# Optimization experiments

Measured on AMD Instinct MI355X. Metric: run time of the kernel, lower is better.

Reference implementation:

```python
import jax, jax.numpy as jnp
import numpy as np

N_NODES = 50000
N_EDGES = 800000
IN_CH, HID, OUT_CH = 128, 256, 40


def setup_inputs() -> dict:
    key = jax.random.key(0)
    ks = jax.random.split(key, 10)
    x = jax.random.normal(ks[0], (N_NODES, IN_CH), dtype=jnp.float32)
    edge_index = jax.random.randint(ks[1], (2, N_EDGES), 0, N_NODES, dtype=jnp.int64)
    s = 0.05  # weight init scale
    return {
        "x": x,
        "edge_index": edge_index,
        "W1a": jax.random.normal(ks[2], (IN_CH, HID), dtype=jnp.float32) * s,
        "b1a": jnp.zeros((HID,), jnp.float32),
        "W2a": jax.random.normal(ks[3], (HID, HID), dtype=jnp.float32) * s,
        "b2a": jnp.zeros((HID,), jnp.float32),
        "W1b": jax.random.normal(ks[4], (HID, HID), dtype=jnp.float32) * s,
        "b1b": jnp.zeros((HID,), jnp.float32),
        "W2b": jax.random.normal(ks[5], (HID, HID), dtype=jnp.float32) * s,
        "b2b": jnp.zeros((HID,), jnp.float32),
        "Wlin": jax.random.normal(ks[6], (HID * 2, OUT_CH), dtype=jnp.float32) * s,
        "blin": jnp.zeros((OUT_CH,), jnp.float32),
    }


def _gin_conv(h, src, dst, W1, b1, W2, b2):
    # sum-aggregate messages h[src] into destination nodes, eps = 0
    agg = jax.ops.segment_sum(h[src], dst, num_segments=N_NODES)
    z = h + agg
    z = jnp.maximum(z @ W1 + b1, 0.0) @ W2 + b2  # 2-layer MLP
    return z


def reference(x, edge_index, W1a, b1a, W2a, b2a, W1b, b1b, W2b, b2b, Wlin, blin):
    src, dst = edge_index[0], edge_index[1]
    h1 = jnp.maximum(_gin_conv(x, src, dst, W1a, b1a, W2a, b2a), 0.0)
    h2 = jnp.maximum(_gin_conv(h1, src, dst, W1b, b1b, W2b, b2b), 0.0)
    h_cat = jnp.concatenate([h1, h2], axis=1)  # [N, 2*HID]
    logits = h_cat @ Wlin + blin
    return jax.nn.log_softmax(logits, axis=1)
```

## Files before the change

### kernel.cpp

```cpp
#include <hip/hip_runtime.h>
#include <math.h>

#define N_NODES 50000
#define N_EDGES 800000
#define IN_CH 128
#define HID 256
#define OUT_CH 40
#define GRP 6250
#define NCHUNK 64
#define TS 264

typedef unsigned short u16;
typedef unsigned char u8;
typedef __attribute__((ext_vector_type(8))) short bf16x8;
typedef __attribute__((ext_vector_type(8))) unsigned short u16x8;
typedef __attribute__((ext_vector_type(4))) float f32x4;
typedef __attribute__((ext_vector_type(2))) float f32x2;

__device__ __forceinline__ float bf2f(u16 u) {
    union { unsigned int i; float f; } v; v.i = ((unsigned int)u) << 16; return v.f;
}
__device__ __forceinline__ u16 f2bf(float f) {
    union { float f; unsigned int i; } v; v.f = f;
    unsigned int x = v.i;
    x += 0x7fffu + ((x >> 16) & 1u);
    return (u16)(x >> 16);
}

#define GLOBAL_AS __attribute__((address_space(1)))
#define LDS_AS __attribute__((address_space(3)))
__device__ __forceinline__ void async_cp16(const void* g, void* l) {
    __builtin_amdgcn_global_load_lds((const GLOBAL_AS unsigned int*)g,
                                     (LDS_AS unsigned int*)l, 16, 0, 0);
}

__device__ __forceinline__ void pack_w(
    const float* __restrict__ in, u16* __restrict__ out, int K, int N, int c)
{
    for (int k = threadIdx.x; k < K; k += 256) {
        int kk32 = k >> 5, quad = (k >> 3) & 3, e = k & 7;
        size_t base = (((size_t)c * (K >> 5) + kk32) * 64 + quad * 16) * 8 + e;
#pragma unroll
        for (int li = 0; li < 16; li++) {
            int n = c * 16 + li;
            float v = (n < N) ? in[(size_t)k * N + n] : 0.f;
            out[base + (size_t)li * 8] = f2bf(v);
        }
    }
}

__global__ __launch_bounds__(256) void prep_fused(
    const float* __restrict__ x, u16* __restrict__ xb, u8* __restrict__ xf8,
    const int* __restrict__ ei, u16* __restrict__ e16,
    const float* __restrict__ W1a, const float* __restrict__ W2a,
    const float* __restrict__ W1b, const float* __restrict__ W2b,
    const float* __restrict__ Wlin,
    u16* __restrict__ W1aPk, u16* __restrict__ W2aPk,
    u16* __restrict__ W1bPk, u16* __restrict__ W2bPk, u16* __restrict__ WlinPk)
{
    int b = blockIdx.x;
    if (b < 6250) {
        int i = b * 256 + threadIdx.x;
        float4 v = ((const float4*)x)[i];
        ushort4 o;
        o.x = f2bf(v.x); o.y = f2bf(v.y); o.z = f2bf(v.z); o.w = f2bf(v.w);
        ((ushort4*)xb)[i] = o;
        int p = __builtin_amdgcn_cvt_pk_fp8_f32(v.x, v.y, 0, false);
        p = __builtin_amdgcn_cvt_pk_fp8_f32(v.z, v.w, p, true);
        ((unsigned int*)xf8)[i] = (unsigned int)p;
    } else if (b < 7813) {
        int i = (b - 6250) * 256 + threadIdx.x;
        if (i < (2 * N_EDGES) / 4) {
            int4 v = ((const int4*)ei)[i];
            ushort4 o;
            o.x = (u16)v.x; o.y = (u16)v.y; o.z = (u16)v.z; o.w = (u16)v.w;
            ((ushort4*)e16)[i] = o;
        }
    } else {
        int t = b - 7813;
        if (t < 16)       pack_w(W1a, W1aPk, IN_CH, HID, t);
        else if (t < 32)  pack_w(W2a, W2aPk, HID, HID, t - 16);
        else if (t < 48)  pack_w(W1b, W1bPk, HID, HID, t - 32);
        else if (t < 64)  pack_w(W2b, W2bPk, HID, HID, t - 48);
        else              pack_w(Wlin, WlinPk, 2 * HID, OUT_CH, t - 64);
    }
}

__global__ __launch_bounds__(256) void hist_priv(
    const u16* __restrict__ dst16, u16* __restrict__ partial)
{
    __shared__ int hist[GRP];
    const int b = blockIdx.x;
    const int g = b & 7;
    const int sub = b >> 3;
    const int lo = g * GRP;
    const int CH = N_EDGES / NCHUNK;
    for (int i = threadIdx.x; i < GRP; i += 256) hist[i] = 0;
    __syncthreads();
    const ushort4* dsts = (const ushort4*)(dst16 + sub * CH);
    for (int k = threadIdx.x; k < CH / 4; k += 256) {
        ushort4 d = dsts[k];
        int r0 = (int)d.x - lo, r1 = (int)d.y - lo;
        int r2 = (int)d.z - lo, r3 = (int)d.w - lo;
        if ((unsigned)r0 < (unsigned)GRP) atomicAdd(&hist[r0], 1);
        if ((unsigned)r1 < (unsigned)GRP) atomicAdd(&hist[r1], 1);
        if ((unsigned)r2 < (unsigned)GRP) atomicAdd(&hist[r2], 1);
        if ((unsigned)r3 < (unsigned)GRP) atomicAdd(&hist[r3], 1);
    }
    __syncthreads();
    u16* po = partial + (size_t)b * GRP;
    for (int i = threadIdx.x; i < GRP; i += 256) po[i] = (u16)hist[i];
}

__global__ __launch_bounds__(256) void scan1(
    const u16* __restrict__ partial, int* __restrict__ excl,
    int* __restrict__ partials_out)
{
    __shared__ int lds[256];
    const int tid = threadIdx.x;
    const int base = blockIdx.x * 1024 + tid * 4;
    int v[4]; int s = 0;
#pragma unroll
    for (int i = 0; i < 4; i++) {
        int idx = base + i;
        int d = 0;
        if (idx < N_NODES) {
            int g = idx / GRP;
            int off = idx - g * GRP;
#pragma unroll
            for (int sub = 0; sub < NCHUNK; sub++)
                d += partial[(size_t)(sub * 8 + g) * GRP + off];
        }
        v[i] = d;
        s += d;
    }
    lds[tid] = s;
    __syncthreads();
    for (int off = 1; off < 256; off <<= 1) {
        int t = (tid >= off) ? lds[tid - off] : 0;
        __syncthreads();
        lds[tid] += t;
        __syncthreads();
    }
    int run = lds[tid] - s;
#pragma unroll
    for (int i = 0; i < 4; i++) {
        int idx = base + i;
        if (idx < N_NODES) excl[idx] = run;
        run += v[i];
    }
    if (tid == 255) partials_out[blockIdx.x] = lds[255];
}

__global__ __launch_bounds__(256) void scan3(
    int* __restrict__ excl, const int* __restrict__ partials,
    int* __restrict__ cursor, int nPart)
{
    __shared__ int bp[64];
    const int tid = threadIdx.x;
    if (tid < 64) {
        int orig = (tid < nPart) ? partials[tid] : 0;
        int v = orig;
#pragma unroll
        for (int off = 1; off < 64; off <<= 1) {
            int t = __shfl_up(v, off, 64);
            if (tid >= off) v += t;
        }
        bp[tid] = v - orig;
    }
    __syncthreads();
    int idx = blockIdx.x * 256 + tid;
    if (idx < N_NODES) {
        int r = excl[idx] + bp[idx >> 10];
        excl[idx] = r;
        cursor[idx] = r;
    }
}

__global__ __launch_bounds__(256) void csr_fill(
    const u16* __restrict__ src16, const u16* __restrict__ dst16,
    int* __restrict__ cursor, u16* __restrict__ csr_src)
{
    const int g = blockIdx.x & 7;
    const int c = blockIdx.x >> 3;
    const int lo = g * GRP, hi = lo + GRP;
    const int base = c * 2048;
#pragma unroll
    for (int i = 0; i < 8; i++) {
        int e = base + i * 256 + threadIdx.x;
        if (e < N_EDGES) {
            int d = dst16[e];
            if (d >= lo && d < hi) {
                int pos = atomicAdd(&cursor[d], 1);
                csr_src[pos] = src16[e];
            }
        }
    }
}

__global__ __launch_bounds__(256) void gather_agg_f8_128(
    const u16* __restrict__ feat_bf, const u8* __restrict__ feat_f8,
    const int* __restrict__ row_ptr, const int* __restrict__ row_end,
    const u16* __restrict__ csr_src, u16* __restrict__ out)
{
    int node = (blockIdx.x * 256 + threadIdx.x) >> 6;
    int lane = threadIdx.x & 63;
    if (node >= N_NODES) return;
    ushort2 sv = ((const ushort2*)(feat_bf + (size_t)node * IN_CH))[lane];
    float ax = bf2f(sv.x), ay = bf2f(sv.y);
    int j = row_ptr[node], e = row_end[node];
    for (; j + 4 <= e; j += 4) {
        int s0 = csr_src[j], s1 = csr_src[j + 1];
        int s2 = csr_src[j + 2], s3 = csr_src[j + 3];
        int v0 = ((const u16*)(feat_f8 + (size_t)s0 * IN_CH))[lane];
        int v1 = ((const u16*)(feat_f8 + (size_t)s1 * IN_CH))[lane];
        int v2 = ((const u16*)(feat_f8 + (size_t)s2 * IN_CH))[lane];
        int v3 = ((const u16*)(feat_f8 + (size_t)s3 * IN_CH))[lane];
        f32x2 d0 = __builtin_amdgcn_cvt_pk_f32_fp8(v0, false);
        f32x2 d1 = __builtin_amdgcn_cvt_pk_f32_fp8(v1, false);
        f32x2 d2 = __builtin_amdgcn_cvt_pk_f32_fp8(v2, false);
        f32x2 d3 = __builtin_amdgcn_cvt_pk_f32_fp8(v3, false);
        ax += (d0.x + d1.x) + (d2.x + d3.x);
        ay += (d0.y + d1.y) + (d2.y + d3.y);
    }
    for (; j < e; j++) {
        int sa = csr_src[j];
        int va = ((const u16*)(feat_f8 + (size_t)sa * IN_CH))[lane];
        f32x2 da = __builtin_amdgcn_cvt_pk_f32_fp8(va, false);
        ax += da.x; ay += da.y;
    }
    ushort2 o; o.x = f2bf(ax); o.y = f2bf(ay);
    ((ushort2*)(out + (size_t)node * IN_CH))[lane] = o;
}

__global__ __launch_bounds__(256) void gather_agg_f8_256(
    const u16* __restrict__ feat_bf, const u8* __restrict__ feat_f8,
    const int* __restrict__ row_ptr, const int* __restrict__ row_end,
    const u16* __restrict__ csr_src, u16* __restrict__ out)
{
    int node = (blockIdx.x * 256 + threadIdx.x) >> 6;
    int lane = threadIdx.x & 63;
    if (node >= N_NODES) return;
    ushort4 sv = ((const ushort4*)(feat_bf + (size_t)node * HID))[lane];
    float ax = bf2f(sv.x), ay = bf2f(sv.y), az = bf2f(sv.z), aw = bf2f(sv.w);
    int j = row_ptr[node], e = row_end[node];
    for (; j + 4 <= e; j += 4) {
        int s0 = csr_src[j], s1 = csr_src[j + 1];
        int s2 = csr_src[j + 2], s3 = csr_src[j + 3];
        int v0 = ((const int*)(feat_f8 + (size_t)s0 * HID))[lane];
        int v1 = ((const int*)(feat_f8 + (size_t)s1 * HID))[lane];
        int v2 = ((const int*)(feat_f8 + (size_t)s2 * HID))[lane];
        int v3 = ((const int*)(feat_f8 + (size_t)s3 * HID))[lane];
        f32x2 l0 = __builtin_amdgcn_cvt_pk_f32_fp8(v0, false);
        f32x2 h0 = __builtin_amdgcn_cvt_pk_f32_fp8(v0, true);
        f32x2 l1 = __builtin_amdgcn_cvt_pk_f32_fp8(v1, false);
        f32x2 h1v = __builtin_amdgcn_cvt_pk_f32_fp8(v1, true);
        f32x2 l2 = __builtin_amdgcn_cvt_pk_f32_fp8(v2, false);
        f32x2 h2v = __builtin_amdgcn_cvt_pk_f32_fp8(v2, true);
        f32x2 l3 = __builtin_amdgcn_cvt_pk_f32_fp8(v3, false);
        f32x2 h3 = __builtin_amdgcn_cvt_pk_f32_fp8(v3, true);
        ax += (l0.x + l1.x) + (l2.x + l3.x);
        ay += (l0.y + l1.y) + (l2.y + l3.y);
        az += (h0.x + h1v.x) + (h2v.x + h3.x);
        aw += (h0.y + h1v.y) + (h2v.y + h3.y);
    }
    for (; j < e; j++) {
        int sa = csr_src[j];
        int va = ((const int*)(feat_f8 + (size_t)sa * HID))[lane];
        f32x2 la = __builtin_amdgcn_cvt_pk_f32_fp8(va, false);
        f32x2 ha = __builtin_amdgcn_cvt_pk_f32_fp8(va, true);
        ax += la.x; ay += la.y; az += ha.x; aw += ha.y;
    }
    ushort4 o;
    o.x = f2bf(ax); o.y = f2bf(ay); o.z = f2bf(az); o.w = f2bf(aw);
    ((ushort4*)(out + (size_t)node * HID))[lane] = o;
}

__global__ __launch_bounds__(256, 4) void mlp_fused(
    const u16* __restrict__ A, int K1,
    const u16* __restrict__ W1pk, const float* __restrict__ b1,
    const u16* __restrict__ W2pk, const float* __restrict__ b2,
    u16* __restrict__ out, u8* __restrict__ outF8, int M)
{
    __shared__ u16 SB[64 * TS];

    const int tid = threadIdx.x;
    const int lane = tid & 63;
    const int wid = tid >> 6;
    const int li = lane & 15;
    const int quad = lane >> 4;
    const int koff = quad * 8;
    const int row0 = blockIdx.x * 64;
    const int KB1 = K1 >> 5;
    const int rsh = (K1 == 256) ? 9 : 8;

    {
        const u8* Ag = (const u8*)(A + (size_t)row0 * K1);
        const int rounds = K1 >> 5;
        for (int j = 0; j < rounds; j++) {
            int L = (j * 256 + tid) * 16;
            int G = L ^ (((L >> rsh) & 7) << 4);
            async_cp16(Ag + G, (u8*)SB + L);
        }
    }

    f32x4 acc[4][4];
#pragma unroll
    for (int i = 0; i < 4; i++)
#pragma unroll
        for (int j = 0; j < 4; j++) acc[i][j] = (f32x4){0.f, 0.f, 0.f, 0.f};

    __syncthreads();

    for (int kk = 0; kk < K1; kk += 32) {
        const int kk32 = kk >> 5;
        bf16x8 af[4], wf[4];
#pragma unroll
        for (int t = 0; t < 4; t++) {
            int row = t * 16 + li;
            int bo = row * (K1 * 2) + (kk + koff) * 2;
            bo ^= (row & 7) << 4;
            af[t] = *(const bf16x8*)((const u8*)SB + bo);
        }
#pragma unroll
        for (int t = 0; t < 4; t++)
            wf[t] = *(const bf16x8*)(W1pk +
                (((size_t)(wid * 4 + t) * KB1 + kk32) * 64 + lane) * 8);
#pragma unroll
        for (int mt = 0; mt < 4; mt++)
#pragma unroll
            for (int nt = 0; nt < 4; nt++)
                acc[mt][nt] = __builtin_amdgcn_mfma_f32_16x16x32_bf16(
                    af[mt], wf[nt], acc[mt][nt], 0, 0, 0);
    }
    __syncthreads();

#pragma unroll
    for (int nt = 0; nt < 4; nt++) {
        int col = wid * 64 + nt * 16 + li;
        float bv = b1[col];
#pragma unroll
        for (int mt = 0; mt < 4; mt++) {
#pragma unroll
            for (int reg = 0; reg < 4; reg++) {
                int row = mt * 16 + quad * 4 + reg;
                float v = fmaxf(acc[mt][nt][reg] + bv, 0.f);
                SB[row * TS + col] = f2bf(v);
                acc[mt][nt][reg] = 0.f;
            }
        }
    }
    __syncthreads();

    for (int kk = 0; kk < HID; kk += 32) {
        const int kk32 = kk >> 5;
        bf16x8 af[4], wf[4];
#pragma unroll
        for (int t = 0; t < 4; t++)
            af[t] = *(const bf16x8*)(SB + (t * 16 + li) * TS + kk + koff);
#pragma unroll
        for (int t = 0; t < 4; t++)
            wf[t] = *(const bf16x8*)(W2pk +
                (((size_t)(wid * 4 + t) * 8 + kk32) * 64 + lane) * 8);
#pragma unroll
        for (int mt = 0; mt < 4; mt++)
#pragma unroll
            for (int nt = 0; nt < 4; nt++)
                acc[mt][nt] = __builtin_amdgcn_mfma_f32_16x16x32_bf16(
                    af[mt], wf[nt], acc[mt][nt], 0, 0, 0);
    }

    __syncthreads();
#pragma unroll
    for (int nt = 0; nt < 4; nt++) {
        int col = wid * 64 + nt * 16 + li;
        float bv = b2[col];
#pragma unroll
        for (int mt = 0; mt < 4; mt++) {
#pragma unroll
            for (int reg = 0; reg < 4; reg++) {
                int row = mt * 16 + quad * 4 + reg;
                float v = fmaxf(acc[mt][nt][reg] + bv, 0.f);
                SB[row * TS + col] = f2bf(v);
            }
        }
    }
    __syncthreads();
#pragma unroll
    for (int it = 0; it < 8; it++) {
        int flat = it * 4096 + tid * 16;
        int r = flat >> 9;
        int cu = (flat & 511) >> 1;
        int row = row0 + r;
        if (row < M) {
            u16x8 v = *(const u16x8*)(SB + r * TS + cu);
            *(u16x8*)(out + (size_t)row * HID + cu) = v;
            if (outF8 != nullptr) {
                int p0 = __builtin_amdgcn_cvt_pk_fp8_f32(bf2f(v[0]), bf2f(v[1]), 0, false);
                p0 = __builtin_amdgcn_cvt_pk_fp8_f32(bf2f(v[2]), bf2f(v[3]), p0, true);
                int p1 = __builtin_amdgcn_cvt_pk_fp8_f32(bf2f(v[4]), bf2f(v[5]), 0, false);
                p1 = __builtin_amdgcn_cvt_pk_fp8_f32(bf2f(v[6]), bf2f(v[7]), p1, true);
                int2 pv; pv.x = p0; pv.y = p1;
                *(int2*)(outF8 + (size_t)row * HID + cu) = pv;
            }
        }
    }
}

__global__ __launch_bounds__(256, 6) void gemm_mfma(
    const u16* __restrict__ A, const u16* __restrict__ Acat, int Ksplit, int ldA,
    const u16* __restrict__ Bpk, const float* __restrict__ bias,
    float* __restrict__ out, int M, int K)
{
    const int tid = threadIdx.x;
    const int lane = tid & 63;
    const int wid = tid >> 6;
    const int li = lane & 15;
    const int quad = lane >> 4;
    const int koff = quad * 8;
    const int row0 = blockIdx.x * 64 + wid * 16;

    f32x4 acc[3];
#pragma unroll
    for (int i = 0; i < 3; i++) acc[i] = (f32x4){0.f, 0.f, 0.f, 0.f};

    int r = row0 + li;
    const int arow = (r < M) ? r : (M - 1);
    const int KB = K >> 5;

#define LD_G(AF, BF, KK)                                                      \
    {   const u16* Ab = ((KK) >= Ksplit) ? Acat : A;                          \
        const int kb = ((KK) >= Ksplit) ? ((KK) - Ksplit) : (KK);             \
        AF = *(const bf16x8*)(Ab + (size_t)arow * ldA + kb + koff);           \
        _Pragma("unroll")                                                     \
        for (int t = 0; t < 3; t++)                                           \
            BF[t] = *(const bf16x8*)(Bpk +                                    \
                (((size_t)t * KB + ((KK) >> 5)) * 64 + lane) * 8); }
#define MFMA3(AF, BF)                                                         \
    {   _Pragma("unroll")                                                     \
        for (int nt = 0; nt < 3; nt++)                                        \
            acc[nt] = __builtin_amdgcn_mfma_f32_16x16x32_bf16(                \
                AF, BF[nt], acc[nt], 0, 0, 0); }

    {
        bf16x8 a0, b0[3], a1, b1v[3];
        LD_G(a0, b0, 0);
        for (int kk = 0; kk < K; kk += 64) {
            LD_G(a1, b1v, kk + 32);
            MFMA3(a0, b0);
            if (kk + 64 < K) LD_G(a0, b0, kk + 64);
            MFMA3(a1, b1v);
        }
    }
#undef LD_G
#undef MFMA3

    float b0v = bias[li];
    float b1s = bias[16 + li];
    float b2s = (li < 8) ? bias[32 + li] : 0.f;
#pragma unroll
    for (int reg = 0; reg < 4; reg++) {
        int row = row0 + quad * 4 + reg;
        float v0 = acc[0][reg] + b0v;
        float v1 = acc[1][reg] + b1s;
        float v2 = (li < 8) ? (acc[2][reg] + b2s) : -INFINITY;
        float m = fmaxf(fmaxf(v0, v1), v2);
#pragma unroll
        for (int off = 1; off < 16; off <<= 1)
            m = fmaxf(m, __shfl_xor(m, off, 64));
        float s = expf(v0 - m) + expf(v1 - m)
                + ((li < 8) ? expf(v2 - m) : 0.f);
#pragma unroll
        for (int off = 1; off < 16; off <<= 1)
            s += __shfl_xor(s, off, 64);
        float lg = m + logf(s);
        if (row < M) {
            out[(size_t)row * OUT_CH + li] = v0 - lg;
            out[(size_t)row * OUT_CH + 16 + li] = v1 - lg;
            if (li < 8) out[(size_t)row * OUT_CH + 32 + li] = v2 - lg;
        }
    }
}

extern "C" void kernel_launch(void* const* d_in, const int* in_sizes, int n_in,
                              void* d_out, int out_size, void* d_ws, size_t ws_size,
                              hipStream_t stream)
{
    const float* x    = (const float*)d_in[0];
    const int*   ei   = (const int*)d_in[1];
    const float* W1a  = (const float*)d_in[2];
    const float* b1a  = (const float*)d_in[3];
    const float* W2a  = (const float*)d_in[4];
    const float* b2a  = (const float*)d_in[5];
    const float* W1b  = (const float*)d_in[6];
    const float* b1b  = (const float*)d_in[7];
    const float* W2b  = (const float*)d_in[8];
    const float* b2b  = (const float*)d_in[9];
    const float* Wlin = (const float*)d_in[10];
    const float* blin = (const float*)d_in[11];
    float* out = (float*)d_out;

    const size_t R = (size_t)N_NODES * HID;
    u16* R0 = (u16*)d_ws;
    u16* R1 = R0 + R;
    u16* R2 = R1 + R;
    u16* R3 = R2 + R;
    u16* R4 = R3 + R;
    u16* xbf = R0;
    u16* zA  = R1;
    u16* partial = (u16*)R1;
    u8*  xf8 = (u8*)(R1 + (size_t)N_NODES * IN_CH);
    u8*  h1f8 = (u8*)R1;
    u16* h1  = R3;
    u16* zB  = R4;
    u16* h2  = R2;

    u16* wts = R4 + R;
    u16* W1aPk = wts;
    u16* W2aPk = W1aPk + 256 * 128;
    u16* W1bPk = W2aPk + 256 * 256;
    u16* W2bPk = W1bPk + 256 * 256;
    u16* WlinPk = W2bPk + 256 * 256;
    int* rowp   = (int*)(WlinPk + 128 * 512);
    int* cursor = rowp + N_NODES;
    int* part   = cursor + N_NODES;
    u16* csr    = (u16*)(part + 64);
    u16* e16    = csr + N_EDGES;
    u16* src16  = e16;
    u16* dst16  = e16 + N_EDGES;

    dim3 blk(256);
    const int scanBlocks = (N_NODES + 1023) / 1024;
    const int aggBlocks  = (N_NODES + 3) / 4;
    const int fillBlocks = 8 * ((N_EDGES + 2047) / 2048);
    const int mlpBlocks  = (N_NODES + 63) / 64;
    const int gemmBlocks = (N_NODES + 63) / 64;

    prep_fused<<<7880, blk, 0, stream>>>(x, xbf, xf8, ei, e16,
                                         W1a, W2a, W1b, W2b, Wlin,
                                         W1aPk, W2aPk, W1bPk, W2bPk, WlinPk);
    hist_priv<<<8 * NCHUNK, blk, 0, stream>>>(dst16, partial);
    scan1<<<scanBlocks, blk, 0, stream>>>(partial, rowp, part);
    scan3<<<(N_NODES + 255) / 256, blk, 0, stream>>>(rowp, part, cursor, scanBlocks);
    csr_fill<<<fillBlocks, blk, 0, stream>>>(src16, dst16, cursor, csr);

    gather_agg_f8_128<<<aggBlocks, blk, 0, stream>>>(xbf, xf8, rowp, cursor, csr, zA);
    mlp_fused<<<mlpBlocks, blk, 0, stream>>>(zA, IN_CH, W1aPk, b1a, W2aPk, b2a,
                                             h1, h1f8, N_NODES);

    gather_agg_f8_256<<<aggBlocks, blk, 0, stream>>>(h1, h1f8, rowp, cursor, csr, zB);
    mlp_fused<<<mlpBlocks, blk, 0, stream>>>(zB, HID, W1bPk, b1b, W2bPk, b2b,
                                             h2, nullptr, N_NODES);

    gemm_mfma<<<gemmBlocks, blk, 0, stream>>>(h1, h2, HID, HID, WlinPk, blin,
                                              out, N_NODES, 2 * HID);
}
```

Baseline: 301.5 us.

## Pack multiple nodes per wavefront in gather-aggregate with wide 16-byte loads

The gather kernels previously gave each node a full 64-lane wave, with each lane reading 2 or 4 bytes per neighbor row. Now each wave handles 8 nodes (128-ch) or 4 nodes (256-ch), and each lane loads 16 fp8 bytes with int4 loads and keeps 16 accumulators. Loops run to the max degree within the wave, with masked loads for shorter rows. The goal is fewer, wider memory transactions and more nodes in flight. The cost is more registers and divergence from uneven degrees across nodes sharing a wave.

```diff
diff --git a/kernel.cpp b/kernel.cpp
--- a/kernel.cpp
+++ b/kernel.cpp
@@ -198,39 +198,63 @@
     }
 }
 
+
 __global__ __launch_bounds__(256) void gather_agg_f8_128(
     const u16* __restrict__ feat_bf, const u8* __restrict__ feat_f8,
     const int* __restrict__ row_ptr, const int* __restrict__ row_end,
     const u16* __restrict__ csr_src, u16* __restrict__ out)
 {
-    int node = (blockIdx.x * 256 + threadIdx.x) >> 6;
-    int lane = threadIdx.x & 63;
-    if (node >= N_NODES) return;
-    ushort2 sv = ((const ushort2*)(feat_bf + (size_t)node * IN_CH))[lane];
-    float ax = bf2f(sv.x), ay = bf2f(sv.y);
-    int j = row_ptr[node], e = row_end[node];
-    for (; j + 4 <= e; j += 4) {
-        int s0 = csr_src[j], s1 = csr_src[j + 1];
-        int s2 = csr_src[j + 2], s3 = csr_src[j + 3];
-        int v0 = ((const u16*)(feat_f8 + (size_t)s0 * IN_CH))[lane];
-        int v1 = ((const u16*)(feat_f8 + (size_t)s1 * IN_CH))[lane];
-        int v2 = ((const u16*)(feat_f8 + (size_t)s2 * IN_CH))[lane];
-        int v3 = ((const u16*)(feat_f8 + (size_t)s3 * IN_CH))[lane];
-        f32x2 d0 = __builtin_amdgcn_cvt_pk_f32_fp8(v0, false);
-        f32x2 d1 = __builtin_amdgcn_cvt_pk_f32_fp8(v1, false);
-        f32x2 d2 = __builtin_amdgcn_cvt_pk_f32_fp8(v2, false);
-        f32x2 d3 = __builtin_amdgcn_cvt_pk_f32_fp8(v3, false);
-        ax += (d0.x + d1.x) + (d2.x + d3.x);
-        ay += (d0.y + d1.y) + (d2.y + d3.y);
-    }
-    for (; j < e; j++) {
-        int sa = csr_src[j];
-        int va = ((const u16*)(feat_f8 + (size_t)sa * IN_CH))[lane];
-        f32x2 da = __builtin_amdgcn_cvt_pk_f32_fp8(va, false);
-        ax += da.x; ay += da.y;
-    }
-    ushort2 o; o.x = f2bf(ax); o.y = f2bf(ay);
-    ((ushort2*)(out + (size_t)node * IN_CH))[lane] = o;
+    const int tid = threadIdx.x;
+    const int lane = tid & 63;
+    const int wv = tid >> 6;
+    const int li = lane & 7;
+    int node = blockIdx.x * 32 + wv * 8 + (lane >> 3);
+    const bool valid = node < N_NODES;
+    if (!valid) node = N_NODES - 1;
+
+    int j = row_ptr[node];
+    int deg = valid ? (row_end[node] - j) : 0;
+
+    float acc[16];
+    {
+        u16x8 s0 = *(const u16x8*)(feat_bf + (size_t)node * IN_CH + li * 16);
+        u16x8 s1 = *(const u16x8*)(feat_bf + (size_t)node * IN_CH + li * 16 + 8);
+#pragma unroll
+        for (int q = 0; q < 8; q++) { acc[q] = bf2f(s0[q]); acc[8 + q] = bf2f(s1[q]); }
+    }
+
+    int maxdeg = deg;
+#pragma unroll
+    for (int off = 8; off < 64; off <<= 1)
+        maxdeg = max(maxdeg, __shfl_xor(maxdeg, off, 64));
+
+    for (int it = 0; it < maxdeg; it += 2) {
+        int4 g0 = {0, 0, 0, 0}, g1 = {0, 0, 0, 0};
+        if (it < deg)
+            g0 = *(const int4*)(feat_f8 + (size_t)csr_src[j + it] * IN_CH + li * 16);
+        if (it + 1 < deg)
+            g1 = *(const int4*)(feat_f8 + (size_t)csr_src[j + it + 1] * IN_CH + li * 16);
+#pragma unroll
+        for (int q = 0; q < 4; q++) {
+            int w0 = (&g0.x)[q], w1 = (&g1.x)[q];
+            f32x2 l0 = __builtin_amdgcn_cvt_pk_f32_fp8(w0, false);
+            f32x2 h0 = __builtin_amdgcn_cvt_pk_f32_fp8(w0, true);
+            f32x2 l1 = __builtin_amdgcn_cvt_pk_f32_fp8(w1, false);
+            f32x2 h1 = __builtin_amdgcn_cvt_pk_f32_fp8(w1, true);
+            acc[q * 4 + 0] += l0.x + l1.x;
+            acc[q * 4 + 1] += l0.y + l1.y;
+            acc[q * 4 + 2] += h0.x + h1.x;
+            acc[q * 4 + 3] += h0.y + h1.y;
+        }
+    }
+
+    if (valid) {
+        u16x8 o0, o1;
+#pragma unroll
+        for (int q = 0; q < 8; q++) { o0[q] = f2bf(acc[q]); o1[q] = f2bf(acc[8 + q]); }
+        *(u16x8*)(out + (size_t)node * IN_CH + li * 16) = o0;
+        *(u16x8*)(out + (size_t)node * IN_CH + li * 16 + 8) = o1;
+    }
 }
 
 __global__ __launch_bounds__(256) void gather_agg_f8_256(
@@ -238,42 +262,53 @@
     const int* __restrict__ row_ptr, const int* __restrict__ row_end,
     const u16* __restrict__ csr_src, u16* __restrict__ out)
 {
-    int node = (blockIdx.x * 256 + threadIdx.x) >> 6;
-    int lane = threadIdx.x & 63;
-    if (node >= N_NODES) return;
-    ushort4 sv = ((const ushort4*)(feat_bf + (size_t)node * HID))[lane];
-    float ax = bf2f(sv.x), ay = bf2f(sv.y), az = bf2f(sv.z), aw = bf2f(sv.w);
-    int j = row_ptr[node], e = row_end[node];
-    for (; j + 4 <= e; j += 4) {
-        int s0 = csr_src[j], s1 = csr_src[j + 1];
-        int s2 = csr_src[j + 2], s3 = csr_src[j + 3];
-        int v0 = ((const int*)(feat_f8 + (size_t)s0 * HID))[lane];
-        int v1 = ((const int*)(feat_f8 + (size_t)s1 * HID))[lane];
-        int v2 = ((const int*)(feat_f8 + (size_t)s2 * HID))[lane];
-        int v3 = ((const int*)(feat_f8 + (size_t)s3 * HID))[lane];
-        f32x2 l0 = __builtin_amdgcn_cvt_pk_f32_fp8(v0, false);
-        f32x2 h0 = __builtin_amdgcn_cvt_pk_f32_fp8(v0, true);
-        f32x2 l1 = __builtin_amdgcn_cvt_pk_f32_fp8(v1, false);
-        f32x2 h1v = __builtin_amdgcn_cvt_pk_f32_fp8(v1, true);
-        f32x2 l2 = __builtin_amdgcn_cvt_pk_f32_fp8(v2, false);
-        f32x2 h2v = __builtin_amdgcn_cvt_pk_f32_fp8(v2, true);
-        f32x2 l3 = __builtin_amdgcn_cvt_pk_f32_fp8(v3, false);
-        f32x2 h3 = __builtin_amdgcn_cvt_pk_f32_fp8(v3, true);
-        ax += (l0.x + l1.x) + (l2.x + l3.x);
-        ay += (l0.y + l1.y) + (l2.y + l3.y);
-        az += (h0.x + h1v.x) + (h2v.x + h3.x);
-        aw += (h0.y + h1v.y) + (h2v.y + h3.y);
-    }
-    for (; j < e; j++) {
-        int sa = csr_src[j];
-        int va = ((const int*)(feat_f8 + (size_t)sa * HID))[lane];
-        f32x2 la = __builtin_amdgcn_cvt_pk_f32_fp8(va, false);
-        f32x2 ha = __builtin_amdgcn_cvt_pk_f32_fp8(va, true);
-        ax += la.x; ay += la.y; az += ha.x; aw += ha.y;
-    }
-    ushort4 o;
-    o.x = f2bf(ax); o.y = f2bf(ay); o.z = f2bf(az); o.w = f2bf(aw);
-    ((ushort4*)(out + (size_t)node * HID))[lane] = o;
+    const int tid = threadIdx.x;
+    const int lane = tid & 63;
+    const int wv = tid >> 6;
+    const int li = lane & 15;
+    const int node = blockIdx.x * 16 + wv * 4 + (lane >> 4);
+
+    int j = row_ptr[node];
+    int deg = row_end[node] - j;
+
+    float acc[16];
+    {
+        u16x8 s0 = *(const u16x8*)(feat_bf + (size_t)node * HID + li * 16);
+        u16x8 s1 = *(const u16x8*)(feat_bf + (size_t)node * HID + li * 16 + 8);
+#pragma unroll
+        for (int q = 0; q < 8; q++) { acc[q] = bf2f(s0[q]); acc[8 + q] = bf2f(s1[q]); }
+    }
+
+    int maxdeg = deg;
+#pragma unroll
+    for (int off = 16; off < 64; off <<= 1)
+        maxdeg = max(maxdeg, __shfl_xor(maxdeg, off, 64));
+
+    for (int it = 0; it < maxdeg; it += 2) {
+        int4 g0 = {0, 0, 0, 0}, g1 = {0, 0, 0, 0};
+        if (it < deg)
+            g0 = *(const int4*)(feat_f8 + (size_t)csr_src[j + it] * HID + li * 16);
+        if (it + 1 < deg)
+            g1 = *(const int4*)(feat_f8 + (size_t)csr_src[j + it + 1] * HID + li * 16);
+#pragma unroll
+        for (int q = 0; q < 4; q++) {
+            int w0 = (&g0.x)[q], w1 = (&g1.x)[q];
+            f32x2 l0 = __builtin_amdgcn_cvt_pk_f32_fp8(w0, false);
+            f32x2 h0 = __builtin_amdgcn_cvt_pk_f32_fp8(w0, true);
+            f32x2 l1 = __builtin_amdgcn_cvt_pk_f32_fp8(w1, false);
+            f32x2 h1 = __builtin_amdgcn_cvt_pk_f32_fp8(w1, true);
+            acc[q * 4 + 0] += l0.x + l1.x;
+            acc[q * 4 + 1] += l0.y + l1.y;
+            acc[q * 4 + 2] += h0.x + h1.x;
+            acc[q * 4 + 3] += h0.y + h1.y;
+        }
+    }
+
+    u16x8 o0, o1;
+#pragma unroll
+    for (int q = 0; q < 8; q++) { o0[q] = f2bf(acc[q]); o1[q] = f2bf(acc[8 + q]); }
+    *(u16x8*)(out + (size_t)node * HID + li * 16) = o0;
+    *(u16x8*)(out + (size_t)node * HID + li * 16 + 8) = o1;
 }
 
 __global__ __launch_bounds__(256, 4) void mlp_fused(
@@ -531,8 +566,9 @@
 
     dim3 blk(256);
     const int scanBlocks = (N_NODES + 1023) / 1024;
-    const int aggBlocks  = (N_NODES + 3) / 4;
     const int fillBlocks = 8 * ((N_EDGES + 2047) / 2048);
+    const int agg128Blocks = (N_NODES + 31) / 32;
+    const int agg256Blocks = N_NODES / 16;
     const int mlpBlocks  = (N_NODES + 63) / 64;
     const int gemmBlocks = (N_NODES + 63) / 64;
 
@@ -544,11 +580,11 @@
     scan3<<<(N_NODES + 255) / 256, blk, 0, stream>>>(rowp, part, cursor, scanBlocks);
     csr_fill<<<fillBlocks, blk, 0, stream>>>(src16, dst16, cursor, csr);
 
-    gather_agg_f8_128<<<aggBlocks, blk, 0, stream>>>(xbf, xf8, rowp, cursor, csr, zA);
+    gather_agg_f8_128<<<agg128Blocks, blk, 0, stream>>>(xbf, xf8, rowp, cursor, csr, zA);
     mlp_fused<<<mlpBlocks, blk, 0, stream>>>(zA, IN_CH, W1aPk, b1a, W2aPk, b2a,
                                              h1, h1f8, N_NODES);
 
-    gather_agg_f8_256<<<aggBlocks, blk, 0, stream>>>(h1, h1f8, rowp, cursor, csr, zB);
+    gather_agg_f8_256<<<agg256Blocks, blk, 0, stream>>>(h1, h1f8, rowp, cursor, csr, zB);
     mlp_fused<<<mlpBlocks, blk, 0, stream>>>(zB, HID, W1bPk, b1b, W2bPk, b2b,
                                              h2, nullptr, N_NODES);
 
```

After: 289.5 us. 4.0% less time.
